# Kernel tuning notes

Measured on AMD Instinct MI355X. Metric: run time of the kernel, lower is better.

## Reference

```python
import jax, jax.numpy as jnp
import numpy as np
from jax import lax

B, C, H, W = 64, 32, 128, 128
E, K = 4, 2
EPS = 1e-5


def setup_inputs() -> dict:
    key = jax.random.key(0)
    ks = jax.random.split(key, 8)
    x = jax.random.normal(ks[0], (B, C, H, W), dtype=jnp.float32)
    weights = jax.random.uniform(ks[1], (B, K), dtype=jnp.float32)
    indices = jax.random.randint(ks[2], (B, K), 0, E, dtype=jnp.int32)
    # stacked per-expert params: conv kernel [E, Co, Ci, 3, 3], BN affine + running stats
    Wc = jax.random.normal(ks[3], (E, C, C, 3, 3), dtype=jnp.float32) * (1.0 / np.sqrt(C * 9))
    gamma = jnp.ones((E, C), dtype=jnp.float32)
    beta = jnp.zeros((E, C), dtype=jnp.float32)
    mean = jax.random.normal(ks[4], (E, C), dtype=jnp.float32) * 0.1
    var = jax.random.uniform(ks[5], (E, C), dtype=jnp.float32) + 0.5
    return {"x": x, "weights": weights, "indices": indices,
            "Wc": Wc, "gamma": gamma, "beta": beta, "mean": mean, "var": var}


def _expert(x, w, g, b, m, v):
    # Conv2d(k=3, s=1, pad=1, no bias) -> BatchNorm2d (inference stats) -> SiLU
    y = lax.conv_general_dilated(x, w, (1, 1), 'SAME',
                                 dimension_numbers=('NCHW', 'OIHW', 'NCHW'))
    scale = (g / jnp.sqrt(v + EPS))[None, :, None, None]
    shift = (b - m * g / jnp.sqrt(v + EPS))[None, :, None, None]
    y = y * scale + shift
    return y * jax.nn.sigmoid(y)  # SiLU


def reference(x, weights, indices, Wc, gamma, beta, mean, var):
    num_experts = Wc.shape[0]
    # combined routing weight per (expert, sample): sum over top-k slots routed to that expert
    onehot = (indices[None, :, :] == jnp.arange(num_experts, dtype=indices.dtype)[:, None, None])  # [E,B,K]
    wcomb = jnp.sum(weights[None, :, :] * onehot.astype(weights.dtype), axis=-1)  # [E,B]
    out = jnp.zeros_like(x)
    for i in range(num_experts):  # small fixed expert count
        y = _expert(x, Wc[i], gamma[i], beta[i], mean[i], var[i])
        out = out + y * wcomb[i][:, None, None, None]
    return out
```

## Files before the change

### kernel.cpp

```cpp
#include <hip/hip_runtime.h>
#include <math.h>


#define B_ 64
#define C_ 32
#define H_ 128
#define W_ 128
#define E_ 4
#define K_ 2
#define EPS_ 1e-5f
#define HW_ (H_ * W_)
#define HP_ 130
#define WP_ 130

#define AROW_B 592
#define A_LDS_B (C_ * AROW_B)
#define XPAD_BYTES ((size_t)B_ * HP_ * WP_ * C_ * 2)
#define AW_OFF   XPAD_BYTES
#define AW_BYTES ((size_t)E_ * A_LDS_B)
#define SCSH_OFF (AW_OFF + AW_BYTES)
#define WS_NEEDED (SCSH_OFF + (size_t)E_ * C_ * 2 * 4)

#define TH 16
#define TW 16

#define LDS_AW   0
#define LDS_SCSH (2 * A_LDS_B)
#define LDS_TOT  (LDS_SCSH + 512)

typedef __attribute__((ext_vector_type(4))) float  f32x4;
typedef __attribute__((ext_vector_type(8))) short  bf16x8;
typedef __attribute__((ext_vector_type(8))) unsigned short u16x8;
typedef __attribute__((ext_vector_type(4))) unsigned short u16x4;

__device__ inline unsigned short f2bf(float f) {
  unsigned u = __builtin_bit_cast(unsigned, f);
  return (unsigned short)((u + 0x7fffu + ((u >> 16) & 1u)) >> 16);
}

__device__ inline void gload16(const void* g, const void* l) {
  __builtin_amdgcn_global_load_lds(
      (const __attribute__((address_space(1))) unsigned int*)g,
      (__attribute__((address_space(3))) unsigned int*)l, 16, 0, 0);
}

__global__ __launch_bounds__(256, 4)
void prep_kernel(const float* __restrict__ x,
                 const float* __restrict__ Wc,
                 const float* __restrict__ gamma,
                 const float* __restrict__ beta,
                 const float* __restrict__ mean,
                 const float* __restrict__ var,
                 unsigned short* __restrict__ wsu) {
  const int bid = blockIdx.x;
  const int tid = threadIdx.x;

  if (bid >= B_ * HP_) {
    int e = bid - B_ * HP_;
    unsigned short* aw = (unsigned short*)((char*)wsu + AW_OFF) + (size_t)e * (A_LDS_B / 2);
    int co  = tid >> 3;
    int ci4 = (tid & 7) * 4;
    const float* wp = Wc + (((size_t)e * C_ + co) * C_ + ci4) * 9;
    float wv[36];
#pragma unroll
    for (int j = 0; j < 36; ++j) wv[j] = wp[j];
    unsigned short* arow = aw + co * (AROW_B / 2) + ci4;
#pragma unroll
    for (int o = 0; o < 9; ++o) {
      u16x4 pk;
#pragma unroll
      for (int q = 0; q < 4; ++q) pk[q] = f2bf(wv[q * 9 + o]);
      *(u16x4*)(arow + o * C_) = pk;
    }
    if (tid < C_) {
      float g  = gamma[e * C_ + tid];
      float bt = beta[e * C_ + tid];
      float mn = mean[e * C_ + tid];
      float vr = var[e * C_ + tid];
      float sc = g * rsqrtf(vr + EPS_);
      float* scsh = (float*)((char*)wsu + SCSH_OFF);
      scsh[(e * C_ + tid) * 2 + 0] = sc;
      scsh[(e * C_ + tid) * 2 + 1] = bt - mn * sc;
    }
    return;
  }

  const int b  = bid / HP_;
  const int hp = bid % HP_;
  unsigned short* xrow = wsu + ((size_t)b * HP_ + hp) * WP_ * C_;

  if (hp == 0 || hp == HP_ - 1) {
    u16x8 z = (u16x8)0;
    for (int c = tid; c < WP_ * C_ / 8; c += 256) *(u16x8*)(xrow + c * 8) = z;
    return;
  }

  __shared__ float tile[C_ * W_];
  const int h = hp - 1;
#pragma unroll
  for (int p = 0; p < 4; ++p) {
    int n  = p * 1024 + tid * 4;
    int c  = n >> 7;
    int px = n & 127;
    *(f32x4*)(tile + n) =
        *(const f32x4*)(x + (((size_t)b * C_ + c) * H_ + h) * W_ + px);
  }
  __syncthreads();

  const int px = tid >> 1;
  const int c0 = (tid & 1) * 16;
  u16x8 o0, o1;
#pragma unroll
  for (int j = 0; j < 8; ++j) o0[j] = f2bf(tile[(c0 + j) * W_ + px]);
#pragma unroll
  for (int j = 0; j < 8; ++j) o1[j] = f2bf(tile[(c0 + 8 + j) * W_ + px]);
  unsigned short* dst = xrow + (px + 1) * C_ + c0;
  *(u16x8*)dst = o0;
  *(u16x8*)(dst + 8) = o1;

  if (tid < 4) {
    int pxb = (tid >> 1) ? (WP_ - 1) : 0;
    int hf  = tid & 1;
    u16x8 z = (u16x8)0;
    unsigned short* d2 = xrow + pxb * C_ + hf * 16;
    *(u16x8*)d2 = z;
    *(u16x8*)(d2 + 8) = z;
  }
}

__global__ __launch_bounds__(256, 3)
void conv_kernel(const unsigned short* __restrict__ xpad,
                 const unsigned short* __restrict__ aw_all,
                 const float* __restrict__ scsh_all,
                 const float* __restrict__ weights,
                 const int* __restrict__ indices,
                 float* __restrict__ out) {
  __shared__ __align__(16) unsigned char lds[LDS_TOT];
  const int tid  = threadIdx.x;
  const int lane = tid & 63;
  const int wid  = tid >> 6;

  const int bid  = blockIdx.x;
  const int xcd  = bid & 7;
  const int ii   = bid >> 3;
  const int b    = (ii >> 6) * 8 + xcd;
  const int tile = ii & 63;
  const int th0  = (tile >> 3) * TH;
  const int tw0  = (tile & 7) * TW;

  const int   e0  = indices[b * K_ + 0];
  const int   e1  = indices[b * K_ + 1];
  const float wk0 = weights[b * K_ + 0];
  const float wk1 = weights[b * K_ + 1];
  const bool  dup = (e0 == e1);
  const float wka = dup ? (wk0 + wk1) : wk0;

  {
    const int nA = (dup ? 1 : 2) * 1184;
    for (int base = wid * 64; base < nA; base += 256) {
      int c = base + lane;
      int e = (c < 1184) ? e0 : e1;
      int r = (c < 1184) ? c : c - 1184;
      const unsigned short* src = aw_all + (size_t)e * (A_LDS_B / 2) + r * 8;
      if (c < nA) gload16(src, lds + LDS_AW + base * 16);
    }
  }
  if (tid < 2 * C_) {
    int s  = tid >> 5;
    int co = tid & 31;
    int e  = s ? e1 : e0;
    float* d = (float*)(lds + LDS_SCSH) + (s * C_ + co) * 2;
    d[0] = scsh_all[(e * C_ + co) * 2 + 0];
    d[1] = scsh_all[(e * C_ + co) * 2 + 1];
  }
  __syncthreads();

  const int lx = lane & 15;
  const int sl = lane >> 4;

  const unsigned short* prow[6];
#pragma unroll
  for (int i = 0; i < 6; ++i)
    prow[i] = xpad + ((size_t)(b * HP_ + th0 + 4 * wid + i) * WP_ + (tw0 + lx)) * C_ + sl * 8;

  f32x4 acc[2][2][4];
#pragma unroll
  for (int s = 0; s < 2; ++s)
#pragma unroll
    for (int m = 0; m < 2; ++m)
#pragma unroll
      for (int j = 0; j < 4; ++j) acc[s][m][j] = (f32x4){0.f, 0.f, 0.f, 0.f};

  bf16x8 F[6];
#pragma unroll
  for (int i = 0; i < 6; ++i) F[i] = *(const bf16x8*)(prow[i]);

#pragma unroll
  for (int dx = 0; dx < 3; ++dx) {
    bf16x8 G[6];
    if (dx < 2) {
#pragma unroll
      for (int i = 0; i < 6; ++i)
        G[i] = *(const bf16x8*)(prow[i] + (dx + 1) * C_);
    }
#pragma unroll
    for (int dy = 0; dy < 3; ++dy) {
      const int o = dy * 3 + dx;
      bf16x8 af0[2], af1[2];
#pragma unroll
      for (int m = 0; m < 2; ++m)
        af0[m] = *(const bf16x8*)(lds + LDS_AW + (m * 16 + lx) * AROW_B + o * 64 + sl * 16);
      if (!dup) {
#pragma unroll
        for (int m = 0; m < 2; ++m)
          af1[m] = *(const bf16x8*)(lds + LDS_AW + A_LDS_B + (m * 16 + lx) * AROW_B + o * 64 + sl * 16);
      }
#pragma unroll
      for (int m = 0; m < 2; ++m)
#pragma unroll
        for (int j = 0; j < 4; ++j)
          acc[0][m][j] = __builtin_amdgcn_mfma_f32_16x16x32_bf16(af0[m], F[j + dy], acc[0][m][j], 0, 0, 0);
      if (!dup) {
#pragma unroll
        for (int m = 0; m < 2; ++m)
#pragma unroll
          for (int j = 0; j < 4; ++j)
            acc[1][m][j] = __builtin_amdgcn_mfma_f32_16x16x32_bf16(af1[m], F[j + dy], acc[1][m][j], 0, 0, 0);
      }
    }
#pragma unroll
    for (int i = 0; i < 6; ++i) F[i] = G[i];
  }

  float res[2][4][4];
#pragma unroll
  for (int m = 0; m < 2; ++m)
#pragma unroll
    for (int j = 0; j < 4; ++j)
#pragma unroll
      for (int r = 0; r < 4; ++r) res[m][j][r] = 0.f;

  const float* scshl = (const float*)(lds + LDS_SCSH);
#pragma unroll
  for (int s = 0; s < 2; ++s) {
    if (s == 1 && dup) break;
    float wk = s ? wk1 : wka;
#pragma unroll
    for (int m = 0; m < 2; ++m)
#pragma unroll
      for (int r = 0; r < 4; ++r) {
        int co = m * 16 + sl * 4 + r;
        float sc = scshl[(s * C_ + co) * 2 + 0];
        float sh = scshl[(s * C_ + co) * 2 + 1];
#pragma unroll
        for (int j = 0; j < 4; ++j) {
          float y = acc[s][m][j][r] * sc + sh;
          float sig = 1.f / (1.f + __expf(-y));
          res[m][j][r] += wk * y * sig;
        }
      }
  }

#pragma unroll
  for (int m = 0; m < 2; ++m)
#pragma unroll
    for (int r = 0; r < 4; ++r) {
      int co = m * 16 + sl * 4 + r;
      float* ob = out + ((size_t)b * C_ + co) * HW_ + (size_t)th0 * W_ + tw0 + lx;
#pragma unroll
      for (int j = 0; j < 4; ++j)
        ob[(size_t)(4 * wid + j) * W_] = res[m][j][r];
    }
}

#define FHALO 18
#define FNPX (FHALO * FHALO)
#define FPX_B 64
#define FIN_LDS_B (FNPX * FPX_B)
#define FSC_OFF (FIN_LDS_B + 2 * A_LDS_B)
#define FLDS_TOTAL (FSC_OFF + 2 * C_ * 8)

__global__ __launch_bounds__(256, 2)
void moe_fallback_kernel(const float* __restrict__ x,
                         const float* __restrict__ weights,
                         const int* __restrict__ indices,
                         const float* __restrict__ Wc,
                         const float* __restrict__ gamma,
                         const float* __restrict__ beta,
                         const float* __restrict__ mean,
                         const float* __restrict__ var,
                         float* __restrict__ out) {
  __shared__ __align__(16) unsigned char lds[FLDS_TOTAL];
  unsigned char* in_t = lds;
  unsigned char* aw0  = lds + FIN_LDS_B;
  unsigned char* aw1  = lds + FIN_LDS_B + A_LDS_B;
  float*         scsh = (float*)(lds + FSC_OFF);

  const int tid = threadIdx.x;
  const int tiles_per_row = W_ / TW;
  const int tiles_per_img = (H_ / TH) * tiles_per_row;
  const int b    = blockIdx.x / tiles_per_img;
  const int tile = blockIdx.x % tiles_per_img;
  const int th0  = (tile / tiles_per_row) * TH;
  const int tw0  = (tile % tiles_per_row) * TW;

  const int   e0  = indices[b * K_ + 0];
  const int   e1  = indices[b * K_ + 1];
  const float wk0 = weights[b * K_ + 0];
  const float wk1 = weights[b * K_ + 1];
  const bool  dup = (e0 == e1);
  const float wka = dup ? (wk0 + wk1) : wk0;

  const float* xb = x + (size_t)b * C_ * HW_;
  for (int i = tid; i < FNPX * 4; i += 256) {
    int px = i % FNPX;
    int cb = i / FNPX;
    int hy = px / FHALO, hx = px % FHALO;
    int gh = th0 + hy - 1, gw = tw0 + hx - 1;
    u16x8 pk = (u16x8)0;
    if (gh >= 0 && gh < H_ && gw >= 0 && gw < W_) {
      const float* src = xb + (size_t)(cb * 8) * HW_ + (size_t)gh * W_ + gw;
#pragma unroll
      for (int j = 0; j < 8; ++j) pk[j] = f2bf(src[(size_t)j * HW_]);
    }
    int slot = cb ^ (px & 3);
    *(u16x8*)(in_t + px * FPX_B + slot * 16) = pk;
  }
  {
    int co  = tid >> 3;
    int ci4 = (tid & 7) * 4;
#pragma unroll
    for (int s = 0; s < 2; ++s) {
      int e = s ? e1 : e0;
      const float* wp = Wc + (size_t)e * C_ * C_ * 9 + (size_t)co * C_ * 9 + (size_t)ci4 * 9;
      float wv[36];
#pragma unroll
      for (int j = 0; j < 36; ++j) wv[j] = wp[j];
      unsigned char* arow = (s ? aw1 : aw0) + co * AROW_B + ci4 * 2;
#pragma unroll
      for (int o = 0; o < 9; ++o) {
        u16x4 pk;
#pragma unroll
        for (int q = 0; q < 4; ++q) pk[q] = f2bf(wv[q * 9 + o]);
        *(u16x4*)(arow + o * 64) = pk;
      }
    }
  }
  if (tid < 64) {
    int s  = tid >> 5;
    int co = tid & 31;
    int e  = s ? e1 : e0;
    float g  = gamma[e * C_ + co];
    float bt = beta[e * C_ + co];
    float mn = mean[e * C_ + co];
    float vr = var[e * C_ + co];
    float sc = g * rsqrtf(vr + EPS_);
    scsh[(s * C_ + co) * 2 + 0] = sc;
    scsh[(s * C_ + co) * 2 + 1] = bt - mn * sc;
  }
  __syncthreads();

  const int lane = tid & 63;
  const int w    = tid >> 6;
  const int lx   = lane & 15;
  const int sl   = lane >> 4;

  f32x4 acc[2][2][4];
#pragma unroll
  for (int s = 0; s < 2; ++s)
#pragma unroll
    for (int m = 0; m < 2; ++m)
#pragma unroll
      for (int j = 0; j < 4; ++j) acc[s][m][j] = (f32x4){0.f, 0.f, 0.f, 0.f};

  int dy = 0, dx = 0;
#pragma unroll 1
  for (int o = 0; o < 9; ++o) {
    bf16x8 bf[4];
#pragma unroll
    for (int j = 0; j < 4; ++j) {
      int hp   = (4 * w + j + dy) * FHALO + (lx + dx);
      int slot = sl ^ (hp & 3);
      bf[j] = *(const bf16x8*)(in_t + hp * FPX_B + slot * 16);
    }
    bf16x8 af0[2], af1[2];
#pragma unroll
    for (int m = 0; m < 2; ++m) {
      int ro = (m * 16 + lx) * AROW_B + o * 64 + sl * 16;
      af0[m] = *(const bf16x8*)(aw0 + ro);
      af1[m] = *(const bf16x8*)(aw1 + ro);
    }
#pragma unroll
    for (int m = 0; m < 2; ++m)
#pragma unroll
      for (int j = 0; j < 4; ++j)
        acc[0][m][j] = __builtin_amdgcn_mfma_f32_16x16x32_bf16(af0[m], bf[j], acc[0][m][j], 0, 0, 0);
    if (!dup) {
#pragma unroll
      for (int m = 0; m < 2; ++m)
#pragma unroll
        for (int j = 0; j < 4; ++j)
          acc[1][m][j] = __builtin_amdgcn_mfma_f32_16x16x32_bf16(af1[m], bf[j], acc[1][m][j], 0, 0, 0);
    }
    if (++dx == 3) { dx = 0; ++dy; }
  }

  float res[2][4][4];
#pragma unroll
  for (int m = 0; m < 2; ++m)
#pragma unroll
    for (int j = 0; j < 4; ++j)
#pragma unroll
      for (int r = 0; r < 4; ++r) res[m][j][r] = 0.f;

#pragma unroll
  for (int s = 0; s < 2; ++s) {
    if (s == 1 && dup) break;
    float wk = s ? wk1 : wka;
#pragma unroll
    for (int m = 0; m < 2; ++m)
#pragma unroll
      for (int r = 0; r < 4; ++r) {
        int co = m * 16 + sl * 4 + r;
        float sc = scsh[(s * C_ + co) * 2 + 0];
        float sh = scsh[(s * C_ + co) * 2 + 1];
#pragma unroll
        for (int j = 0; j < 4; ++j) {
          float y = acc[s][m][j][r] * sc + sh;
          float sig = 1.f / (1.f + __expf(-y));
          res[m][j][r] += wk * y * sig;
        }
      }
  }
#pragma unroll
  for (int m = 0; m < 2; ++m)
#pragma unroll
    for (int r = 0; r < 4; ++r) {
      int co = m * 16 + sl * 4 + r;
      float* ob = out + ((size_t)b * C_ + co) * HW_ + (size_t)th0 * W_ + tw0 + lx;
#pragma unroll
      for (int j = 0; j < 4; ++j)
        ob[(size_t)(4 * w + j) * W_] = res[m][j][r];
    }
}

extern "C" void kernel_launch(void* const* d_in, const int* in_sizes, int n_in,
                              void* d_out, int out_size, void* d_ws, size_t ws_size,
                              hipStream_t stream) {
  const float* x       = (const float*)d_in[0];
  const float* weights = (const float*)d_in[1];
  const int*   indices = (const int*)d_in[2];
  const float* Wc      = (const float*)d_in[3];
  const float* gamma   = (const float*)d_in[4];
  const float* beta    = (const float*)d_in[5];
  const float* mean    = (const float*)d_in[6];
  const float* var     = (const float*)d_in[7];
  float* out = (float*)d_out;

  if (d_ws != nullptr && ws_size >= WS_NEEDED) {
    unsigned short* wsu = (unsigned short*)d_ws;
    const unsigned short* aw_all   = (const unsigned short*)((char*)d_ws + AW_OFF);
    const float*          scsh_all = (const float*)((char*)d_ws + SCSH_OFF);
    prep_kernel<<<B_ * HP_ + E_, 256, 0, stream>>>(x, Wc, gamma, beta, mean, var, wsu);
    conv_kernel<<<B_ * 64, 256, 0, stream>>>(wsu, aw_all, scsh_all, weights, indices, out);
  } else {
    moe_fallback_kernel<<<B_ * 64, 256, 0, stream>>>(
        x, weights, indices, Wc, gamma, beta, mean, var, out);
  }
}
```

Measured before the change: 104.9 us.

## Swap MFMA operand roles so pixels are rows, enabling vectorized output stores

The conv kernel now feeds pixel activations as the MFMA A operand and weights as B, so each lane's accumulator holds four consecutive output pixels for one channel. Output stores become 16-byte float4 writes instead of scalar strided stores. Tiles change from 16x16 pixel blocks to 8-row by 32-column strips, with each wave covering 2 rows by 32 columns. The input loop is reordered to stream rows (dy outer) while reusing two resident rows. Register pressure and the halo-load pattern change, which may affect occupancy.

Result: slower. 109.0 us (+3.9%).

```diff
diff --git a/kernel.cpp b/kernel.cpp
--- a/kernel.cpp
+++ b/kernel.cpp
@@ -20,9 +20,6 @@
 #define AW_BYTES ((size_t)E_ * A_LDS_B)
 #define SCSH_OFF (AW_OFF + AW_BYTES)
 #define WS_NEEDED (SCSH_OFF + (size_t)E_ * C_ * 2 * 4)
-
-#define TH 16
-#define TW 16
 
 #define LDS_AW   0
 #define LDS_SCSH (2 * A_LDS_B)
@@ -145,8 +142,10 @@
   const int ii   = bid >> 3;
   const int b    = (ii >> 6) * 8 + xcd;
   const int tile = ii & 63;
-  const int th0  = (tile >> 3) * TH;
-  const int tw0  = (tile & 7) * TW;
+  const int rowg = tile >> 2;
+  const int cseg = tile & 3;
+  const int r0   = rowg * 8 + wid * 2;
+  const int c0   = cseg * 32;
 
   const int   e0  = indices[b * K_ + 0];
   const int   e1  = indices[b * K_ + 1];
@@ -178,99 +177,104 @@
   const int lx = lane & 15;
   const int sl = lane >> 4;
 
-  const unsigned short* prow[6];
-#pragma unroll
-  for (int i = 0; i < 6; ++i)
-    prow[i] = xpad + ((size_t)(b * HP_ + th0 + 4 * wid + i) * WP_ + (tw0 + lx)) * C_ + sl * 8;
-
-  f32x4 acc[2][2][4];
+  const unsigned short* base =
+      xpad + ((size_t)(b * HP_ + r0) * WP_ + c0 + lx) * C_ + sl * 8;
+
+  auto loadrow = [&](bf16x8* dst, int hr) {
+#pragma unroll
+    for (int s = 0; s < 6; ++s)
+      dst[s] = *(const bf16x8*)(base + ((size_t)hr * WP_ + (s / 3) * 16 + (s % 3)) * C_);
+  };
+
+  f32x4 acc[2][4][2];
 #pragma unroll
   for (int s = 0; s < 2; ++s)
 #pragma unroll
-    for (int m = 0; m < 2; ++m)
-#pragma unroll
-      for (int j = 0; j < 4; ++j) acc[s][m][j] = (f32x4){0.f, 0.f, 0.f, 0.f};
-
-  bf16x8 F[6];
-#pragma unroll
-  for (int i = 0; i < 6; ++i) F[i] = *(const bf16x8*)(prow[i]);
-
-#pragma unroll
-  for (int dx = 0; dx < 3; ++dx) {
-    bf16x8 G[6];
-    if (dx < 2) {
-#pragma unroll
-      for (int i = 0; i < 6; ++i)
-        G[i] = *(const bf16x8*)(prow[i] + (dx + 1) * C_);
-    }
-#pragma unroll
-    for (int dy = 0; dy < 3; ++dy) {
+    for (int mt = 0; mt < 4; ++mt)
+#pragma unroll
+      for (int nc = 0; nc < 2; ++nc) acc[s][mt][nc] = (f32x4){0.f, 0.f, 0.f, 0.f};
+
+  bf16x8 FA[6], FB[6];
+  loadrow(FA, 0);
+  loadrow(FB, 1);
+
+#pragma unroll
+  for (int dy = 0; dy < 3; ++dy) {
+    bf16x8 FC[6];
+    if (dy < 2) loadrow(FC, dy + 2);
+
+#pragma unroll
+    for (int dx = 0; dx < 3; ++dx) {
       const int o = dy * 3 + dx;
-      bf16x8 af0[2], af1[2];
-#pragma unroll
-      for (int m = 0; m < 2; ++m)
-        af0[m] = *(const bf16x8*)(lds + LDS_AW + (m * 16 + lx) * AROW_B + o * 64 + sl * 16);
+      bf16x8 bf0[2], bf1[2];
+#pragma unroll
+      for (int nc = 0; nc < 2; ++nc)
+        bf0[nc] = *(const bf16x8*)(lds + LDS_AW + (nc * 16 + lx) * AROW_B + o * 64 + sl * 16);
       if (!dup) {
 #pragma unroll
-        for (int m = 0; m < 2; ++m)
-          af1[m] = *(const bf16x8*)(lds + LDS_AW + A_LDS_B + (m * 16 + lx) * AROW_B + o * 64 + sl * 16);
+        for (int nc = 0; nc < 2; ++nc)
+          bf1[nc] = *(const bf16x8*)(lds + LDS_AW + A_LDS_B + (nc * 16 + lx) * AROW_B + o * 64 + sl * 16);
       }
 #pragma unroll
-      for (int m = 0; m < 2; ++m)
-#pragma unroll
-        for (int j = 0; j < 4; ++j)
-          acc[0][m][j] = __builtin_amdgcn_mfma_f32_16x16x32_bf16(af0[m], F[j + dy], acc[0][m][j], 0, 0, 0);
-      if (!dup) {
-#pragma unroll
-        for (int m = 0; m < 2; ++m)
-#pragma unroll
-          for (int j = 0; j < 4; ++j)
-            acc[1][m][j] = __builtin_amdgcn_mfma_f32_16x16x32_bf16(af1[m], F[j + dy], acc[1][m][j], 0, 0, 0);
-      }
-    }
-#pragma unroll
-    for (int i = 0; i < 6; ++i) F[i] = G[i];
-  }
-
-  float res[2][4][4];
-#pragma unroll
-  for (int m = 0; m < 2; ++m)
-#pragma unroll
-    for (int j = 0; j < 4; ++j)
-#pragma unroll
-      for (int r = 0; r < 4; ++r) res[m][j][r] = 0.f;
+      for (int j = 0; j < 2; ++j)
+#pragma unroll
+        for (int m2 = 0; m2 < 2; ++m2) {
+          bf16x8 A = j ? FB[m2 * 3 + dx] : FA[m2 * 3 + dx];
+#pragma unroll
+          for (int nc = 0; nc < 2; ++nc)
+            acc[0][j * 2 + m2][nc] =
+                __builtin_amdgcn_mfma_f32_16x16x32_bf16(A, bf0[nc], acc[0][j * 2 + m2][nc], 0, 0, 0);
+          if (!dup) {
+#pragma unroll
+            for (int nc = 0; nc < 2; ++nc)
+              acc[1][j * 2 + m2][nc] =
+                  __builtin_amdgcn_mfma_f32_16x16x32_bf16(A, bf1[nc], acc[1][j * 2 + m2][nc], 0, 0, 0);
+          }
+        }
+    }
+#pragma unroll
+    for (int s = 0; s < 6; ++s) { FA[s] = FB[s]; FB[s] = FC[s]; }
+  }
 
   const float* scshl = (const float*)(lds + LDS_SCSH);
+  f32x4 res[4][2];
+#pragma unroll
+  for (int mt = 0; mt < 4; ++mt)
+#pragma unroll
+    for (int nc = 0; nc < 2; ++nc) res[mt][nc] = (f32x4){0.f, 0.f, 0.f, 0.f};
+
 #pragma unroll
   for (int s = 0; s < 2; ++s) {
     if (s == 1 && dup) break;
     float wk = s ? wk1 : wka;
 #pragma unroll
-    for (int m = 0; m < 2; ++m)
-#pragma unroll
-      for (int r = 0; r < 4; ++r) {
-        int co = m * 16 + sl * 4 + r;
-        float sc = scshl[(s * C_ + co) * 2 + 0];
-        float sh = scshl[(s * C_ + co) * 2 + 1];
-#pragma unroll
-        for (int j = 0; j < 4; ++j) {
-          float y = acc[s][m][j][r] * sc + sh;
+    for (int nc = 0; nc < 2; ++nc) {
+      int co = nc * 16 + lx;
+      float sc = scshl[(s * C_ + co) * 2 + 0];
+      float sh = scshl[(s * C_ + co) * 2 + 1];
+#pragma unroll
+      for (int mt = 0; mt < 4; ++mt) {
+#pragma unroll
+        for (int r = 0; r < 4; ++r) {
+          float y = acc[s][mt][nc][r] * sc + sh;
           float sig = 1.f / (1.f + __expf(-y));
-          res[m][j][r] += wk * y * sig;
+          res[mt][nc][r] += wk * y * sig;
         }
       }
-  }
-
-#pragma unroll
-  for (int m = 0; m < 2; ++m)
-#pragma unroll
-    for (int r = 0; r < 4; ++r) {
-      int co = m * 16 + sl * 4 + r;
-      float* ob = out + ((size_t)b * C_ + co) * HW_ + (size_t)th0 * W_ + tw0 + lx;
-#pragma unroll
-      for (int j = 0; j < 4; ++j)
-        ob[(size_t)(4 * wid + j) * W_] = res[m][j][r];
-    }
+    }
+  }
+
+#pragma unroll
+  for (int j = 0; j < 2; ++j)
+#pragma unroll
+    for (int m2 = 0; m2 < 2; ++m2)
+#pragma unroll
+      for (int nc = 0; nc < 2; ++nc) {
+        int co = nc * 16 + lx;
+        float* ob = out + ((size_t)b * C_ + co) * HW_ +
+                    (size_t)(r0 + j) * W_ + c0 + m2 * 16 + sl * 4;
+        *(f32x4*)ob = res[j * 2 + m2][nc];
+      }
 }
 
 #define FHALO 18
@@ -279,6 +283,8 @@
 #define FIN_LDS_B (FNPX * FPX_B)
 #define FSC_OFF (FIN_LDS_B + 2 * A_LDS_B)
 #define FLDS_TOTAL (FSC_OFF + 2 * C_ * 8)
+#define TH 16
+#define TW 16
 
 __global__ __launch_bounds__(256, 2)
 void moe_fallback_kernel(const float* __restrict__ x,
```
